# Performance work log

Measured on AMD Instinct MI355X. Metric: run time of the kernel, lower is better.

The kernel has to match this reference:

```python
import jax, jax.numpy as jnp
import numpy as np

B, N, C, H, P = 8, 4096, 256, 4, 64  # batch, tokens, hidden, heads, proj_size


def setup_inputs() -> dict:
    key = jax.random.key(0)
    ks = jax.random.split(key, 6)
    sc = 0.02
    x = jax.random.normal(ks[0], (B, N, C), jnp.float32)
    bank = jax.random.normal(ks[1], (B, N, C), jnp.float32)  # unused by forward, kept for fidelity
    W_qkvv = jax.random.normal(ks[2], (4 * C, C), jnp.float32) * sc  # Linear(C, 4C), no bias
    W_E = jax.random.normal(ks[3], (P, N), jnp.float32) * sc          # E = F shared Linear(N, P)
    b_E = jnp.zeros((P,), jnp.float32)
    temperature = jnp.ones((H, 1, 1), jnp.float32)
    temperature2 = jnp.ones((H, 1, 1), jnp.float32)
    W_out1 = jax.random.normal(ks[4], (C // 2, C), jnp.float32) * sc  # out_proj (spatial branch)
    b_out1 = jnp.zeros((C // 2,), jnp.float32)
    W_out2 = jax.random.normal(ks[5], (C // 2, C), jnp.float32) * sc  # out_proj2 (channel branch)
    b_out2 = jnp.zeros((C // 2,), jnp.float32)
    prelu_a = jnp.array(0.25, jnp.float32)  # nn.PReLU() default: single shared slope
    return {"x": x, "bank": bank, "W_qkvv": W_qkvv, "W_E": W_E, "b_E": b_E,
            "temperature": temperature, "temperature2": temperature2,
            "W_out1": W_out1, "b_out1": b_out1, "W_out2": W_out2, "b_out2": b_out2,
            "prelu_a": prelu_a}


def _l2norm(t):
    # torch F.normalize(dim=-1): x / max(||x||_2, eps)
    return t / jnp.maximum(jnp.linalg.norm(t, axis=-1, keepdims=True), 1e-12)


def reference(x, bank, W_qkvv, W_E, b_E, temperature, temperature2,
              W_out1, b_out1, W_out2, b_out2, prelu_a):
    Bb, Nn, Cc = x.shape
    Hh = temperature.shape[0]
    d = Cc // Hh
    # qkvv projection -> [4, B, H, N, d], then transpose token/feature axes -> [B, H, d, N]
    qkvv = (x @ W_qkvv.T).reshape(Bb, Nn, 4, Hh, d).transpose(2, 0, 3, 1, 4)
    q, k, v_ca, v_sa = (qkvv[0].transpose(0, 1, 3, 2), qkvv[1].transpose(0, 1, 3, 2),
                        qkvv[2].transpose(0, 1, 3, 2), qkvv[3].transpose(0, 1, 3, 2))
    # shared linear E=F projects the token axis N -> P (applied to UNnormalized k, v_sa)
    k_proj = jnp.einsum('bhdn,pn->bhdp', k, W_E) + b_E      # [B,H,d,P]
    v_sa_proj = jnp.einsum('bhdn,pn->bhdp', v_sa, W_E) + b_E  # [B,H,d,P]
    qn = _l2norm(q)
    kn = _l2norm(k)
    # channel attention: [B,H,d,d]
    attn_ca = jax.nn.softmax(jnp.einsum('bhdn,bhen->bhde', qn, kn) * temperature, axis=-1)
    x_ca = jnp.einsum('bhde,bhen->bhdn', attn_ca, v_ca).transpose(0, 3, 1, 2).reshape(Bb, Nn, Cc)
    # spatial attention (projected): [B,H,N,P]
    attn_sa = jax.nn.softmax(jnp.einsum('bhdn,bhdp->bhnp', qn, k_proj) * temperature2, axis=-1)
    x_sa = jnp.einsum('bhnp,bhdp->bhnd', attn_sa, v_sa_proj).transpose(0, 2, 1, 3).reshape(Bb, Nn, Cc)
    x_sa = x_sa @ W_out1.T + b_out1
    x_ca = x_ca @ W_out2.T + b_out2
    out = jnp.concatenate([x_sa, x_ca], axis=-1)
    return jnp.where(out >= 0, out, prelu_a * out)  # PReLU
```

## Files before the change

kernel.cpp:

```cpp
#include <hip/hip_runtime.h>
#include <cstdint>
#include <cstddef>

constexpr int B_ = 8, N_ = 4096, C_ = 256, H_ = 4, D_ = 64, P_ = 64;
constexpr int OC_ = 4 * C_;
constexpr int M_  = B_ * N_;
constexpr int GX_ROWS = 320;
constexpr int KSPLIT_G = 16;

#define DEV_INLINE __device__ __forceinline__

typedef unsigned short ushort_t;
typedef __attribute__((ext_vector_type(8))) short short8;
typedef __attribute__((ext_vector_type(4))) short short4v;
typedef __attribute__((ext_vector_type(4))) float floatx4;

DEV_INLINE short f2bf(float f) {
  unsigned int u = __builtin_bit_cast(unsigned int, f);
  u += 0x7FFFu + ((u >> 16) & 1u);
  return (short)(u >> 16);
}
DEV_INLINE float bf2f(ushort_t u) {
  return __builtin_bit_cast(float, (unsigned int)u << 16);
}
DEV_INLINE short4v cvt4(float4 v) {
  short4v s = {f2bf(v.x), f2bf(v.y), f2bf(v.z), f2bf(v.w)};
  return s;
}

__global__ __launch_bounds__(512) void k_qv(const float* __restrict__ x,
                                            const float* __restrict__ Wq,
                                            const float* __restrict__ WE,
                                            const float* __restrict__ W1,
                                            const float* __restrict__ W2,
                                            ushort_t* __restrict__ xb,
                                            ushort_t* __restrict__ wqb,
                                            ushort_t* __restrict__ web,
                                            ushort_t* __restrict__ w1b,
                                            ushort_t* __restrict__ w2b,
                                            ushort_t* __restrict__ qv) {
  __shared__ __align__(16) short As[128 * 72];
  __shared__ __align__(16) short Bs[256 * 72];
  const int cs = blockIdx.y;
  const int t = threadIdx.x;
  if (cs == 2) {
    constexpr size_t WQ4 = 65536, WE4 = 65536, W14 = 8192;
    constexpr size_t TOTW4 = WQ4 + WE4 + 2 * W14;
    for (size_t i = (size_t)blockIdx.x * 512 + t; i < TOTW4; i += (size_t)256 * 512) {
      const float* src; ushort_t* dst; size_t o;
      if (i < WQ4) { src = Wq; dst = wqb; o = i; }
      else if (i < WQ4 + WE4) { src = WE; dst = web; o = i - WQ4; }
      else if (i < WQ4 + WE4 + W14) { src = W1; dst = w1b; o = i - WQ4 - WE4; }
      else { src = W2; dst = w2b; o = i - WQ4 - WE4 - W14; }
      float4 v = ((const float4*)src)[o];
      *(short4v*)&dst[o * 4] = cvt4(v);
    }
    return;
  }
  const int bm = blockIdx.x * 128;
  const int wbase = cs ? 512 : 0;
  const int c = (t & 15) * 4;
  const int row = t >> 4;
  const int lane = t & 63, wave = t >> 6;
  const int m16 = lane & 15, quad = lane >> 4;
  const int wm = (wave >> 2) << 6, wn = (wave & 3) << 6;
  floatx4 acc[4][4];
#pragma unroll
  for (int i = 0; i < 4; ++i)
#pragma unroll
    for (int j = 0; j < 4; ++j) acc[i][j] = (floatx4)(0.f);
#pragma unroll 1
  for (int k0 = 0; k0 < 256; k0 += 64) {
    float4 av[4], bv[8];
#pragma unroll
    for (int rep = 0; rep < 4; ++rep)
      av[rep] = *(const float4*)&x[(size_t)(bm + row + 32 * rep) * 256 + k0 + c];
#pragma unroll
    for (int rep = 0; rep < 8; ++rep)
      bv[rep] = *(const float4*)&Wq[(size_t)(wbase + row + 32 * rep) * 256 + k0 + c];
    __syncthreads();
#pragma unroll
    for (int rep = 0; rep < 4; ++rep) {
      short4v s = cvt4(av[rep]);
      *(short4v*)&As[(row + 32 * rep) * 72 + c] = s;
      if (cs == 0)
        *(short4v*)&xb[(size_t)(bm + row + 32 * rep) * 256 + k0 + c] = s;
    }
#pragma unroll
    for (int rep = 0; rep < 8; ++rep)
      *(short4v*)&Bs[(row + 32 * rep) * 72 + c] = cvt4(bv[rep]);
    __syncthreads();
#pragma unroll
    for (int ks = 0; ks < 2; ++ks) {
      short8 af[4], bf[4];
#pragma unroll
      for (int i = 0; i < 4; ++i)
        af[i] = *(const short8*)&As[(wm + i * 16 + m16) * 72 + ks * 32 + quad * 8];
#pragma unroll
      for (int j = 0; j < 4; ++j)
        bf[j] = *(const short8*)&Bs[(wn + j * 16 + m16) * 72 + ks * 32 + quad * 8];
#pragma unroll
      for (int i = 0; i < 4; ++i)
#pragma unroll
        for (int j = 0; j < 4; ++j)
          acc[i][j] = __builtin_amdgcn_mfma_f32_16x16x32_bf16(af[i], bf[j], acc[i][j], 0, 0, 0);
    }
  }
#pragma unroll
  for (int i = 0; i < 4; ++i)
#pragma unroll
    for (int r = 0; r < 4; ++r) {
      const int gr = bm + wm + i * 16 + quad * 4 + r;
#pragma unroll
      for (int j = 0; j < 4; ++j)
        qv[(size_t)gr * 512 + cs * 256 + wn + j * 16 + m16] =
            (ushort_t)f2bf(acc[i][j][r]);
    }
}

__global__ __launch_bounds__(512) void k_gram(const ushort_t* __restrict__ xb,
                                              const ushort_t* __restrict__ web,
                                              float* __restrict__ Gx) {
  __shared__ __align__(16) short Bs[256 * 64];
  __shared__ __align__(16) short Ws[64 * 64];
  const int job = blockIdx.x;
  const int b = blockIdx.y >> 4;
  const int ksp = blockIdx.y & 15;
  const int t = threadIdx.x;
  const int lane = t & 63, wave = t >> 6;
  const int m16 = lane & 15, quad = lane >> 4;
  const int wm = (wave >> 2) << 6;
  const int wn4 = (wave & 3) << 6;
  const int wn2 = wave << 5;
  const int c0 = (t & 63) * 4;
  const int tp = t >> 6;
  floatx4 acc[4][4];
#pragma unroll
  for (int i = 0; i < 4; ++i)
#pragma unroll
    for (int j = 0; j < 4; ++j) acc[i][j] = (floatx4)(0.f);
#pragma unroll 1
  for (int it = 0; it < 4; ++it) {
    const int n0 = ksp * (N_ / KSPLIT_G) + it * 64;
    __syncthreads();
#pragma unroll
    for (int q = 0; q < 4; ++q) {
      const int tok = q * 16 + 2 * tp;
      const size_t r0 = (size_t)(b * N_ + n0 + tok) * C_ + c0;
      short4v aa = *(const short4v*)&xb[r0];
      short4v cc = *(const short4v*)&xb[r0 + C_];
#pragma unroll
      for (int ii = 0; ii < 4; ++ii) {
        const int r = c0 + ii;
        const int col = tok ^ (8 * ((r >> 3) & 7));
        unsigned int w = (unsigned int)(ushort_t)aa[ii] |
                         ((unsigned int)(ushort_t)cc[ii] << 16);
        *(unsigned int*)&Bs[r * 64 + col] = w;
      }
    }
    if (job == 2) {
      const int oc8 = (t & 7) * 8;
      const int p0 = t >> 3;
      short8 v = *(const short8*)&web[(size_t)p0 * N_ + n0 + oc8];
      *(short8*)&Ws[p0 * 64 + (oc8 ^ (8 * ((p0 >> 3) & 7)))] = v;
    }
    __syncthreads();
#pragma unroll
    for (int ks = 0; ks < 2; ++ks) {
      const int boct = ks * 32 + quad * 8;
      if (job < 2) {
        short8 af[4], bf[4];
#pragma unroll
        for (int i = 0; i < 4; ++i) {
          const int rA = job * 128 + wm + 16 * i + m16;
          af[i] = *(const short8*)&Bs[rA * 64 + (boct ^ (8 * ((rA >> 3) & 7)))];
        }
#pragma unroll
        for (int j = 0; j < 4; ++j) {
          const int rB = wn4 + 16 * j + m16;
          bf[j] = *(const short8*)&Bs[rB * 64 + (boct ^ (8 * ((rB >> 3) & 7)))];
        }
#pragma unroll
        for (int i = 0; i < 4; ++i)
#pragma unroll
          for (int j = 0; j < 4; ++j)
            acc[i][j] = __builtin_amdgcn_mfma_f32_16x16x32_bf16(af[i], bf[j], acc[i][j], 0, 0, 0);
      } else {
        short8 af[4], bf[2];
#pragma unroll
        for (int i = 0; i < 4; ++i) {
          const int rA = 16 * i + m16;
          af[i] = *(const short8*)&Ws[rA * 64 + (boct ^ (8 * ((rA >> 3) & 7)))];
        }
#pragma unroll
        for (int j = 0; j < 2; ++j) {
          const int rB = wn2 + 16 * j + m16;
          bf[j] = *(const short8*)&Bs[rB * 64 + (boct ^ (8 * ((rB >> 3) & 7)))];
        }
#pragma unroll
        for (int i = 0; i < 4; ++i)
#pragma unroll
          for (int j = 0; j < 2; ++j)
            acc[i][j] = __builtin_amdgcn_mfma_f32_16x16x32_bf16(af[i], bf[j], acc[i][j], 0, 0, 0);
      }
    }
  }
  if (job < 2) {
#pragma unroll
    for (int i = 0; i < 4; ++i)
#pragma unroll
      for (int r = 0; r < 4; ++r) {
        const int grow = job * 128 + wm + 16 * i + quad * 4 + r;
        const size_t rowoff = ((size_t)b * GX_ROWS + grow) * 256;
#pragma unroll
        for (int j = 0; j < 4; ++j)
          atomicAdd(&Gx[rowoff + wn4 + 16 * j + m16], acc[i][j][r]);
      }
  } else {
#pragma unroll
    for (int i = 0; i < 4; ++i)
#pragma unroll
      for (int r = 0; r < 4; ++r) {
        const int grow = 256 + 16 * i + quad * 4 + r;
        const size_t rowoff = ((size_t)b * GX_ROWS + grow) * 256;
#pragma unroll
        for (int j = 0; j < 2; ++j)
          atomicAdd(&Gx[rowoff + wn2 + 16 * j + m16], acc[i][j][r]);
      }
  }
}

__global__ __launch_bounds__(256) void k_mid1(const ushort_t* __restrict__ wqb,
                                              const float* __restrict__ Gx,
                                              ushort_t* __restrict__ T2b,
                                              float* __restrict__ ssq) {
  __shared__ __align__(16) short As[128 * 72];
  __shared__ __align__(16) short Bs[128 * 72];
  const int bm = blockIdx.x * 128;
  const int b  = blockIdx.y >> 1;
  const int jb = blockIdx.y & 1;
  const int t = threadIdx.x;
  const int oc = t & 7;
  const int rr = t >> 3;
  const int lane = t & 63, wave = t >> 6;
  const int m16 = lane & 15, quad = lane >> 4;
  const int wm = (wave >> 1) << 6, wn = (wave & 1) << 6;
  const float* Bsrc = Gx + ((size_t)b * GX_ROWS + jb * 128) * 256;
  floatx4 acc[4][4];
#pragma unroll
  for (int i = 0; i < 4; ++i)
#pragma unroll
    for (int j = 0; j < 4; ++j) acc[i][j] = (floatx4)(0.f);
#pragma unroll 1
  for (int k0 = 0; k0 < 256; k0 += 64) {
    short8 a8[4], b8[4];
#pragma unroll
    for (int j = 0; j < 4; ++j) {
      const int r = rr + 32 * j;
      a8[j] = *(const short8*)&wqb[(size_t)(bm + r) * 256 + k0 + 8 * oc];
      float4 g0 = *(const float4*)&Bsrc[(size_t)r * 256 + k0 + 8 * oc];
      float4 g1 = *(const float4*)&Bsrc[(size_t)r * 256 + k0 + 8 * oc + 4];
      short8 bb;
      bb[0] = f2bf(g0.x); bb[1] = f2bf(g0.y); bb[2] = f2bf(g0.z); bb[3] = f2bf(g0.w);
      bb[4] = f2bf(g1.x); bb[5] = f2bf(g1.y); bb[6] = f2bf(g1.z); bb[7] = f2bf(g1.w);
      b8[j] = bb;
    }
    __syncthreads();
#pragma unroll
    for (int j = 0; j < 4; ++j) {
      const int r = rr + 32 * j;
      *(short8*)&As[r * 72 + 8 * oc] = a8[j];
      *(short8*)&Bs[r * 72 + 8 * oc] = b8[j];
    }
    __syncthreads();
#pragma unroll
    for (int ks = 0; ks < 2; ++ks) {
      short8 af[4], bf[4];
#pragma unroll
      for (int i = 0; i < 4; ++i)
        af[i] = *(const short8*)&As[(wm + i * 16 + m16) * 72 + ks * 32 + quad * 8];
#pragma unroll
      for (int j = 0; j < 4; ++j)
        bf[j] = *(const short8*)&Bs[(wn + j * 16 + m16) * 72 + ks * 32 + quad * 8];
#pragma unroll
      for (int i = 0; i < 4; ++i)
#pragma unroll
        for (int j = 0; j < 4; ++j)
          acc[i][j] = __builtin_amdgcn_mfma_f32_16x16x32_bf16(af[i], bf[j], acc[i][j], 0, 0, 0);
    }
  }
#pragma unroll
  for (int i = 0; i < 4; ++i)
#pragma unroll
    for (int r = 0; r < 4; ++r) {
      const int gr = bm + wm + i * 16 + quad * 4 + r;
      float s = 0.f;
#pragma unroll
      for (int j = 0; j < 4; ++j) {
        const int col = jb * 128 + wn + j * 16 + m16;
        T2b[((size_t)b * 512 + gr) * 256 + col] = (ushort_t)f2bf(acc[i][j][r]);
        s += bf2f(wqb[(size_t)gr * 256 + col]) * acc[i][j][r];
      }
      s += __shfl_xor(s, 1);
      s += __shfl_xor(s, 2);
      s += __shfl_xor(s, 4);
      s += __shfl_xor(s, 8);
      if (m16 == 0) atomicAdd(&ssq[b * 512 + gr], s);
    }
}

__global__ __launch_bounds__(64) void k_mid2(const ushort_t* __restrict__ wqb,
                                             const ushort_t* __restrict__ T2b,
                                             const float* __restrict__ Gx,
                                             const float* __restrict__ ssq,
                                             const float* __restrict__ bE,
                                             const float* __restrict__ t1,
                                             const float* __restrict__ t2,
                                             ushort_t* __restrict__ ab,
                                             ushort_t* __restrict__ ksb,
                                             ushort_t* __restrict__ vsb) {
  const int bh = blockIdx.x;
  const int job = blockIdx.y;
  const int b = bh >> 2, h = bh & 3;
  const int lane = threadIdx.x & 63;
  const int m16 = lane & 15, quad = lane >> 4;
  const int Abase = (job == 0 ? 0 : (job == 1 ? 256 : 768)) + h * 64;
  floatx4 acc[4][4];
#pragma unroll
  for (int i = 0; i < 4; ++i)
#pragma unroll
    for (int j = 0; j < 4; ++j) acc[i][j] = (floatx4)(0.f);
#pragma unroll
  for (int ks = 0; ks < 8; ++ks) {
    const int boct = ks * 32 + quad * 8;
    short8 af[4], bf[4];
#pragma unroll
    for (int i = 0; i < 4; ++i)
      af[i] = *(const short8*)&wqb[(size_t)(Abase + 16 * i + m16) * 256 + boct];
    if (job == 0) {
#pragma unroll
      for (int j = 0; j < 4; ++j)
        bf[j] = *(const short8*)&T2b[((size_t)b * 512 + 256 + h * 64 + 16 * j + m16) * 256 + boct];
    } else {
#pragma unroll
      for (int j = 0; j < 4; ++j) {
        const float* gp = Gx + ((size_t)b * GX_ROWS + 256 + 16 * j + m16) * 256 + boct;
        float4 g0 = *(const float4*)gp;
        float4 g1 = *(const float4*)(gp + 4);
        short8 bb;
        bb[0] = f2bf(g0.x); bb[1] = f2bf(g0.y); bb[2] = f2bf(g0.z); bb[3] = f2bf(g0.w);
        bb[4] = f2bf(g1.x); bb[5] = f2bf(g1.y); bb[6] = f2bf(g1.z); bb[7] = f2bf(g1.w);
        bf[j] = bb;
      }
    }
#pragma unroll
    for (int i = 0; i < 4; ++i)
#pragma unroll
      for (int j = 0; j < 4; ++j)
        acc[i][j] = __builtin_amdgcn_mfma_f32_16x16x32_bf16(af[i], bf[j], acc[i][j], 0, 0, 0);
  }
  if (job == 0) {
    const float t1h = t1[h];
    float rnk[4];
#pragma unroll
    for (int j = 0; j < 4; ++j)
      rnk[j] = 1.f / fmaxf(sqrtf(ssq[b * 512 + 256 + h * 64 + 16 * j + m16]), 1e-12f);
#pragma unroll
    for (int i = 0; i < 4; ++i)
#pragma unroll
      for (int r = 0; r < 4; ++r) {
        const int d = 16 * i + quad * 4 + r;
        const float rq = 1.f / fmaxf(sqrtf(ssq[b * 512 + h * 64 + d]), 1e-12f);
        float l[4];
        float m = -1e30f;
#pragma unroll
        for (int j = 0; j < 4; ++j) {
          l[j] = acc[i][j][r] * rq * rnk[j] * t1h;
          m = fmaxf(m, l[j]);
        }
        m = fmaxf(m, __shfl_xor(m, 1));
        m = fmaxf(m, __shfl_xor(m, 2));
        m = fmaxf(m, __shfl_xor(m, 4));
        m = fmaxf(m, __shfl_xor(m, 8));
        float s = 0.f;
#pragma unroll
        for (int j = 0; j < 4; ++j) {
          l[j] = __expf(l[j] - m);
          s += l[j];
        }
        s += __shfl_xor(s, 1);
        s += __shfl_xor(s, 2);
        s += __shfl_xor(s, 4);
        s += __shfl_xor(s, 8);
        const float inv = 1.f / s;
#pragma unroll
        for (int j = 0; j < 4; ++j)
          ab[(size_t)bh * 4096 + d * 64 + 16 * j + m16] = (ushort_t)f2bf(l[j] * inv);
      }
  } else if (job == 1) {
    const float tt = t2[h];
#pragma unroll
    for (int i = 0; i < 4; ++i)
#pragma unroll
      for (int r = 0; r < 4; ++r) {
        const int d = 16 * i + quad * 4 + r;
        const float rq = 1.f / fmaxf(sqrtf(ssq[b * 512 + h * 64 + d]), 1e-12f);
#pragma unroll
        for (int j = 0; j < 4; ++j) {
          const int p = 16 * j + m16;
          ksb[(size_t)bh * 4096 + p * 64 + d] =
              (ushort_t)f2bf((acc[i][j][r] + bE[p]) * rq * tt);
        }
      }
  } else {
#pragma unroll
    for (int i = 0; i < 4; ++i)
#pragma unroll
      for (int r = 0; r < 4; ++r) {
        const int d = 16 * i + quad * 4 + r;
#pragma unroll
        for (int j = 0; j < 4; ++j) {
          const int p = 16 * j + m16;
          vsb[(size_t)bh * 4096 + d * 64 + p] = (ushort_t)f2bf(acc[i][j][r] + bE[p]);
        }
      }
  }
}

__global__ __launch_bounds__(256) void k_attn(const ushort_t* __restrict__ qv,
                                              const ushort_t* __restrict__ ab,
                                              const ushort_t* __restrict__ ksb,
                                              const ushort_t* __restrict__ vsb,
                                              ushort_t* __restrict__ x_ca,
                                              ushort_t* __restrict__ x_sa) {
  __shared__ float Pl[64][68];
  const int bh = blockIdx.x;
  const int b = bh >> 2, h = bh & 3;
  const int lane = threadIdx.x & 63, wave = threadIdx.x >> 6;
  const int m16 = lane & 15, quad = lane >> 4;
  if (blockIdx.y < 32) {
    const int n0 = blockIdx.y * 128;
    const ushort_t* abb = ab + (size_t)bh * 4096;
    short8 bf[2][4];
#pragma unroll
    for (int ks = 0; ks < 2; ++ks)
#pragma unroll
      for (int j = 0; j < 4; ++j)
        bf[ks][j] = *(const short8*)&abb[(16 * j + m16) * 64 + ks * 32 + quad * 8];
#pragma unroll
    for (int mm = 0; mm < 2; ++mm) {
      const int tokbase = n0 + 64 * mm + 16 * wave;
      const ushort_t* vrow =
          qv + (size_t)(b * N_ + tokbase + m16) * 512 + 256 + h * 64 + quad * 8;
      short8 af0 = *(const short8*)&vrow[0];
      short8 af1 = *(const short8*)&vrow[32];
      floatx4 o[4];
#pragma unroll
      for (int j = 0; j < 4; ++j) o[j] = (floatx4)(0.f);
#pragma unroll
      for (int j = 0; j < 4; ++j) {
        o[j] = __builtin_amdgcn_mfma_f32_16x16x32_bf16(af0, bf[0][j], o[j], 0, 0, 0);
        o[j] = __builtin_amdgcn_mfma_f32_16x16x32_bf16(af1, bf[1][j], o[j], 0, 0, 0);
      }
#pragma unroll
      for (int j = 0; j < 4; ++j)
#pragma unroll
        for (int r = 0; r < 4; ++r)
          x_ca[(size_t)(b * N_ + tokbase + quad * 4 + r) * C_ + h * 64 + 16 * j + m16] =
              (ushort_t)f2bf(o[j][r]);
    }
    return;
  }
  const int n0 = (blockIdx.y - 32) * 64;
  const ushort_t* qrow =
      qv + (size_t)(b * N_ + n0 + 16 * wave + m16) * 512 + h * 64 + quad * 8;
  short8 qf0 = *(const short8*)&qrow[0];
  short8 qf1 = *(const short8*)&qrow[32];
  const ushort_t* kb = ksb + (size_t)bh * 4096;
  const ushort_t* vb = vsb + (size_t)bh * 4096;
  short8 kf[2][4], vf[2][4];
#pragma unroll
  for (int ks = 0; ks < 2; ++ks)
#pragma unroll
    for (int j = 0; j < 4; ++j) {
      kf[ks][j] = *(const short8*)&kb[(16 * j + m16) * 64 + ks * 32 + quad * 8];
      vf[ks][j] = *(const short8*)&vb[(16 * j + m16) * 64 + ks * 32 + quad * 8];
    }
  floatx4 s[4];
#pragma unroll
  for (int j = 0; j < 4; ++j) s[j] = (floatx4)(0.f);
#pragma unroll
  for (int j = 0; j < 4; ++j) {
    s[j] = __builtin_amdgcn_mfma_f32_16x16x32_bf16(qf0, kf[0][j], s[j], 0, 0, 0);
    s[j] = __builtin_amdgcn_mfma_f32_16x16x32_bf16(qf1, kf[1][j], s[j], 0, 0, 0);
  }
  float p[4][4];
#pragma unroll
  for (int r = 0; r < 4; ++r) {
    float mr = fmaxf(fmaxf(s[0][r], s[1][r]), fmaxf(s[2][r], s[3][r]));
    mr = fmaxf(mr, __shfl_xor(mr, 1));
    mr = fmaxf(mr, __shfl_xor(mr, 2));
    mr = fmaxf(mr, __shfl_xor(mr, 4));
    mr = fmaxf(mr, __shfl_xor(mr, 8));
    float sr = 0.f;
#pragma unroll
    for (int j = 0; j < 4; ++j) {
      const float e = __expf(s[j][r] - mr);
      p[j][r] = e;
      sr += e;
    }
    sr += __shfl_xor(sr, 1);
    sr += __shfl_xor(sr, 2);
    sr += __shfl_xor(sr, 4);
    sr += __shfl_xor(sr, 8);
    const float inv = 1.f / sr;
#pragma unroll
    for (int j = 0; j < 4; ++j) p[j][r] *= inv;
  }
#pragma unroll
  for (int j = 0; j < 4; ++j)
#pragma unroll
    for (int r = 0; r < 4; ++r)
      Pl[16 * wave + quad * 4 + r][16 * j + m16] = p[j][r];
  __syncthreads();
  short8 pf[2];
#pragma unroll
  for (int ks = 0; ks < 2; ++ks) {
    float4 x0 = *(const float4*)&Pl[16 * wave + m16][ks * 32 + quad * 8];
    float4 x1 = *(const float4*)&Pl[16 * wave + m16][ks * 32 + quad * 8 + 4];
    short8 v;
    v[0] = f2bf(x0.x); v[1] = f2bf(x0.y); v[2] = f2bf(x0.z); v[3] = f2bf(x0.w);
    v[4] = f2bf(x1.x); v[5] = f2bf(x1.y); v[6] = f2bf(x1.z); v[7] = f2bf(x1.w);
    pf[ks] = v;
  }
  floatx4 o[4];
#pragma unroll
  for (int j = 0; j < 4; ++j) o[j] = (floatx4)(0.f);
#pragma unroll
  for (int j = 0; j < 4; ++j) {
    o[j] = __builtin_amdgcn_mfma_f32_16x16x32_bf16(pf[0], vf[0][j], o[j], 0, 0, 0);
    o[j] = __builtin_amdgcn_mfma_f32_16x16x32_bf16(pf[1], vf[1][j], o[j], 0, 0, 0);
  }
#pragma unroll
  for (int j = 0; j < 4; ++j)
#pragma unroll
    for (int r = 0; r < 4; ++r)
      x_sa[(size_t)(b * N_ + n0 + 16 * wave + quad * 4 + r) * C_ + h * 64 + 16 * j + m16] =
          (ushort_t)f2bf(o[j][r]);
}

__global__ __launch_bounds__(256) void k_out_mfma(const ushort_t* __restrict__ xsa,
                                                  const ushort_t* __restrict__ xca,
                                                  const ushort_t* __restrict__ w1b,
                                                  const float* __restrict__ b1,
                                                  const ushort_t* __restrict__ w2b,
                                                  const float* __restrict__ b2,
                                                  const float* __restrict__ pa,
                                                  float* __restrict__ out) {
  __shared__ __align__(16) short As[128 * 72];
  __shared__ __align__(16) short Bs[128 * 72];
  const int bm = blockIdx.x * 128;
  const int half = blockIdx.y;
  const ushort_t* A = half ? xca : xsa;
  const ushort_t* W = half ? w2b : w1b;
  const float* bias = half ? b2 : b1;
  const int t = threadIdx.x;
  const int oc = t & 7;
  const int rr = t >> 3;
  const int lane = t & 63, wave = t >> 6;
  const int m16 = lane & 15, quad = lane >> 4;
  const int wm = (wave >> 1) << 6, wn = (wave & 1) << 6;
  floatx4 acc[4][4];
#pragma unroll
  for (int i = 0; i < 4; ++i)
#pragma unroll
    for (int j = 0; j < 4; ++j) acc[i][j] = (floatx4)(0.f);
#pragma unroll 1
  for (int k0 = 0; k0 < 256; k0 += 64) {
    short8 a8[4], b8[4];
#pragma unroll
    for (int j = 0; j < 4; ++j) {
      const int r = rr + 32 * j;
      a8[j] = *(const short8*)&A[(size_t)(bm + r) * 256 + k0 + 8 * oc];
      b8[j] = *(const short8*)&W[(size_t)r * 256 + k0 + 8 * oc];
    }
    __syncthreads();
#pragma unroll
    for (int j = 0; j < 4; ++j) {
      const int r = rr + 32 * j;
      *(short8*)&As[r * 72 + 8 * oc] = a8[j];
      *(short8*)&Bs[r * 72 + 8 * oc] = b8[j];
    }
    __syncthreads();
#pragma unroll
    for (int ks = 0; ks < 2; ++ks) {
      short8 af[4], bf[4];
#pragma unroll
      for (int i = 0; i < 4; ++i)
        af[i] = *(const short8*)&As[(wm + i * 16 + m16) * 72 + ks * 32 + quad * 8];
#pragma unroll
      for (int j = 0; j < 4; ++j)
        bf[j] = *(const short8*)&Bs[(wn + j * 16 + m16) * 72 + ks * 32 + quad * 8];
#pragma unroll
      for (int i = 0; i < 4; ++i)
#pragma unroll
        for (int j = 0; j < 4; ++j)
          acc[i][j] = __builtin_amdgcn_mfma_f32_16x16x32_bf16(af[i], bf[j], acc[i][j], 0, 0, 0);
    }
  }
  const float slope = pa[0];
  float bj[4];
#pragma unroll
  for (int j = 0; j < 4; ++j) bj[j] = bias[wn + j * 16 + m16];
#pragma unroll
  for (int i = 0; i < 4; ++i)
#pragma unroll
    for (int r = 0; r < 4; ++r) {
      const int gr = bm + wm + i * 16 + quad * 4 + r;
#pragma unroll
      for (int j = 0; j < 4; ++j) {
        float v = acc[i][j][r] + bj[j];
        v = v >= 0.f ? v : slope * v;
        out[(size_t)gr * C_ + half * 128 + wn + j * 16 + m16] = v;
      }
    }
}

extern "C" void kernel_launch(void* const* d_in, const int* in_sizes, int n_in,
                              void* d_out, int out_size, void* d_ws, size_t ws_size,
                              hipStream_t stream) {
  (void)in_sizes; (void)n_in; (void)out_size; (void)ws_size;
  const float* x  = (const float*)d_in[0];
  const float* Wq = (const float*)d_in[2];
  const float* WE = (const float*)d_in[3];
  const float* bE = (const float*)d_in[4];
  const float* t1 = (const float*)d_in[5];
  const float* t2 = (const float*)d_in[6];
  const float* W1 = (const float*)d_in[7];
  const float* b1 = (const float*)d_in[8];
  const float* W2 = (const float*)d_in[9];
  const float* b2 = (const float*)d_in[10];
  const float* pa = (const float*)d_in[11];
  float* out = (float*)d_out;

  float* ws = (float*)d_ws;
  size_t off = 0;
  float* Gx  = ws + off; off += (size_t)B_ * GX_ROWS * 256;
  float* ssq = ws + off; off += (size_t)B_ * 512;
  ushort_t* qv  = (ushort_t*)(ws + off); off += (size_t)M_ * 512 / 2;
  ushort_t* xsa = (ushort_t*)(ws + off); off += (size_t)M_ * C_ / 2;
  ushort_t* xca = (ushort_t*)(ws + off); off += (size_t)M_ * C_ / 2;
  ushort_t* ksb = (ushort_t*)(ws + off); off += 32 * 4096 / 2;
  ushort_t* vsb = (ushort_t*)(ws + off); off += 32 * 4096 / 2;
  ushort_t* ab  = (ushort_t*)(ws + off); off += 32 * 4096 / 2;
  ushort_t* xb  = (ushort_t*)(ws + off); off += (size_t)M_ * C_ / 2;
  ushort_t* wqb = (ushort_t*)(ws + off); off += (size_t)OC_ * C_ / 2;
  ushort_t* w1b = (ushort_t*)(ws + off); off += (size_t)128 * C_ / 2;
  ushort_t* w2b = (ushort_t*)(ws + off); off += (size_t)128 * C_ / 2;
  ushort_t* web = (ushort_t*)(ws + off); off += (size_t)P_ * N_ / 2;
  ushort_t* T2b = (ushort_t*)(ws + off); off += (size_t)B_ * 512 * C_ / 2;

  hipMemsetAsync(Gx, 0, ((size_t)B_ * GX_ROWS * 256 + B_ * 512) * sizeof(float), stream);

  k_qv<<<dim3(M_ / 128, 3), 512, 0, stream>>>(x, Wq, WE, W1, W2,
                                              xb, wqb, web, w1b, w2b, qv);
  k_gram<<<dim3(3, B_ * KSPLIT_G), 512, 0, stream>>>(xb, web, Gx);
  k_mid1<<<dim3(4, B_ * 2), 256, 0, stream>>>(wqb, Gx, T2b, ssq);
  k_mid2<<<dim3(32, 3), 64, 0, stream>>>(wqb, T2b, Gx, ssq, bE, t1, t2, ab, ksb, vsb);
  k_attn<<<dim3(32, 96), 256, 0, stream>>>(qv, ab, ksb, vsb, xca, xsa);
  k_out_mfma<<<dim3(M_ / 128, 2), 256, 0, stream>>>(xsa, xca, w1b, b1, w2b, b2, pa, out);
}
```

Before: 255.8 us.

## Split cast/transpose kernel, use transposed bf16 x for gram, replace atomics with partial reduction

Adds a separate cast kernel that converts x to bf16 and also writes a channel-major transposed copy, plus converts the weights. The qv GEMM and gram GEMM then read bf16 directly with 16-byte loads instead of converting fp32 or doing in-LDS transposes. Gram split-K now writes per-split partials that a new reduction kernel sums, replacing global float atomics and the large memset. The cost is an extra kernel launch, an extra full bf16 copy of x written and read, and a larger workspace for the partials.

```diff
diff --git a/kernel.cpp b/kernel.cpp
--- a/kernel.cpp
+++ b/kernel.cpp
@@ -6,7 +6,8 @@
 constexpr int OC_ = 4 * C_;
 constexpr int M_  = B_ * N_;
 constexpr int GX_ROWS = 320;
-constexpr int KSPLIT_G = 16;
+constexpr int KS_G = 8;
+constexpr int XT_TILES = M_ / 64;
 
 #define DEV_INLINE __device__ __forceinline__
 
@@ -28,25 +29,25 @@
   return s;
 }
 
-__global__ __launch_bounds__(512) void k_qv(const float* __restrict__ x,
-                                            const float* __restrict__ Wq,
-                                            const float* __restrict__ WE,
-                                            const float* __restrict__ W1,
-                                            const float* __restrict__ W2,
-                                            ushort_t* __restrict__ xb,
-                                            ushort_t* __restrict__ wqb,
-                                            ushort_t* __restrict__ web,
-                                            ushort_t* __restrict__ w1b,
-                                            ushort_t* __restrict__ w2b,
-                                            ushort_t* __restrict__ qv) {
-  __shared__ __align__(16) short As[128 * 72];
-  __shared__ __align__(16) short Bs[256 * 72];
-  const int cs = blockIdx.y;
+__global__ __launch_bounds__(256) void k_cast(const float* __restrict__ x,
+                                              const float* __restrict__ Wq,
+                                              const float* __restrict__ WE,
+                                              const float* __restrict__ W1,
+                                              const float* __restrict__ W2,
+                                              ushort_t* __restrict__ xb,
+                                              ushort_t* __restrict__ xt,
+                                              ushort_t* __restrict__ wqb,
+                                              ushort_t* __restrict__ web,
+                                              ushort_t* __restrict__ w1b,
+                                              ushort_t* __restrict__ w2b) {
   const int t = threadIdx.x;
-  if (cs == 2) {
-    constexpr size_t WQ4 = 65536, WE4 = 65536, W14 = 8192;
+  if (blockIdx.x >= XT_TILES) {
+    constexpr size_t WQ4 = (size_t)OC_ * C_ / 4;
+    constexpr size_t WE4 = (size_t)P_ * N_ / 4;
+    constexpr size_t W14 = (size_t)128 * C_ / 4;
     constexpr size_t TOTW4 = WQ4 + WE4 + 2 * W14;
-    for (size_t i = (size_t)blockIdx.x * 512 + t; i < TOTW4; i += (size_t)256 * 512) {
+    const size_t stride = (size_t)128 * 256;
+    for (size_t i = (size_t)(blockIdx.x - XT_TILES) * 256 + t; i < TOTW4; i += stride) {
       const float* src; ushort_t* dst; size_t o;
       if (i < WQ4) { src = Wq; dst = wqb; o = i; }
       else if (i < WQ4 + WE4) { src = WE; dst = web; o = i - WQ4; }
@@ -57,10 +58,40 @@
     }
     return;
   }
+  __shared__ __align__(16) short Xs[64 * 264];
+  const int n0 = blockIdx.x * 64;
+  const int b = n0 >> 12, nl = n0 & 4095;
+#pragma unroll
+  for (int rep = 0; rep < 16; ++rep) {
+    const int f4 = rep * 256 + t;
+    const int row = f4 >> 6, c4 = f4 & 63;
+    float4 v = *(const float4*)&x[(size_t)(n0 + row) * 256 + c4 * 4];
+    short4v s = cvt4(v);
+    *(short4v*)&xb[(size_t)(n0 + row) * 256 + c4 * 4] = s;
+    *(short4v*)&Xs[row * 264 + c4 * 4] = s;
+  }
+  __syncthreads();
+  const int ch = t;
+  ushort_t* dst = &xt[((size_t)b * 256 + ch) * 4096 + nl];
+#pragma unroll
+  for (int g = 0; g < 8; ++g) {
+    short8 o;
+#pragma unroll
+    for (int i = 0; i < 8; ++i) o[i] = Xs[(g * 8 + i) * 264 + ch];
+    *(short8*)&dst[g * 8] = o;
+  }
+}
+
+__global__ __launch_bounds__(512) void k_qv(const ushort_t* __restrict__ xb,
+                                            const ushort_t* __restrict__ wqb,
+                                            ushort_t* __restrict__ qv) {
+  __shared__ __align__(16) short As[128 * 72];
+  __shared__ __align__(16) short Bs[256 * 72];
   const int bm = blockIdx.x * 128;
-  const int wbase = cs ? 512 : 0;
-  const int c = (t & 15) * 4;
-  const int row = t >> 4;
+  const int y = blockIdx.y;
+  const int wrow = y ? 512 : 0;
+  const int t = threadIdx.x;
+  const int oc = t & 7, rr = t >> 3;
   const int lane = t & 63, wave = t >> 6;
   const int m16 = lane & 15, quad = lane >> 4;
   const int wm = (wave >> 2) << 6, wn = (wave & 3) << 6;
@@ -71,24 +102,20 @@
     for (int j = 0; j < 4; ++j) acc[i][j] = (floatx4)(0.f);
 #pragma unroll 1
   for (int k0 = 0; k0 < 256; k0 += 64) {
-    float4 av[4], bv[8];
-#pragma unroll
-    for (int rep = 0; rep < 4; ++rep)
-      av[rep] = *(const float4*)&x[(size_t)(bm + row + 32 * rep) * 256 + k0 + c];
-#pragma unroll
-    for (int rep = 0; rep < 8; ++rep)
-      bv[rep] = *(const float4*)&Wq[(size_t)(wbase + row + 32 * rep) * 256 + k0 + c];
+    short8 a8[2], b8[4];
+#pragma unroll
+    for (int rp = 0; rp < 2; ++rp)
+      a8[rp] = *(const short8*)&xb[(size_t)(bm + rr + 64 * rp) * 256 + k0 + 8 * oc];
+#pragma unroll
+    for (int rp = 0; rp < 4; ++rp)
+      b8[rp] = *(const short8*)&wqb[(size_t)(wrow + rr + 64 * rp) * 256 + k0 + 8 * oc];
     __syncthreads();
 #pragma unroll
-    for (int rep = 0; rep < 4; ++rep) {
-      short4v s = cvt4(av[rep]);
-      *(short4v*)&As[(row + 32 * rep) * 72 + c] = s;
-      if (cs == 0)
-        *(short4v*)&xb[(size_t)(bm + row + 32 * rep) * 256 + k0 + c] = s;
-    }
-#pragma unroll
-    for (int rep = 0; rep < 8; ++rep)
-      *(short4v*)&Bs[(row + 32 * rep) * 72 + c] = cvt4(bv[rep]);
+    for (int rp = 0; rp < 2; ++rp)
+      *(short8*)&As[(rr + 64 * rp) * 72 + 8 * oc] = a8[rp];
+#pragma unroll
+    for (int rp = 0; rp < 4; ++rp)
+      *(short8*)&Bs[(rr + 64 * rp) * 72 + 8 * oc] = b8[rp];
     __syncthreads();
 #pragma unroll
     for (int ks = 0; ks < 2; ++ks) {
@@ -113,73 +140,63 @@
       const int gr = bm + wm + i * 16 + quad * 4 + r;
 #pragma unroll
       for (int j = 0; j < 4; ++j)
-        qv[(size_t)gr * 512 + cs * 256 + wn + j * 16 + m16] =
+        qv[(size_t)gr * 512 + y * 256 + wn + j * 16 + m16] =
             (ushort_t)f2bf(acc[i][j][r]);
     }
 }
 
-__global__ __launch_bounds__(512) void k_gram(const ushort_t* __restrict__ xb,
+__global__ __launch_bounds__(512) void k_gram(const ushort_t* __restrict__ xt,
                                               const ushort_t* __restrict__ web,
-                                              float* __restrict__ Gx) {
-  __shared__ __align__(16) short Bs[256 * 64];
-  __shared__ __align__(16) short Ws[64 * 64];
+                                              float* __restrict__ Gxp) {
+  __shared__ __align__(16) short As[128 * 72];
+  __shared__ __align__(16) short Bs[256 * 72];
   const int job = blockIdx.x;
-  const int b = blockIdx.y >> 4;
-  const int ksp = blockIdx.y & 15;
+  const int y = blockIdx.y;
+  const int b = y >> 3, ksp = y & 7;
   const int t = threadIdx.x;
+  const int oc = t & 7, rr = t >> 3;
   const int lane = t & 63, wave = t >> 6;
   const int m16 = lane & 15, quad = lane >> 4;
-  const int wm = (wave >> 2) << 6;
-  const int wn4 = (wave & 3) << 6;
-  const int wn2 = wave << 5;
-  const int c0 = (t & 63) * 4;
-  const int tp = t >> 6;
+  const int wm = (wave >> 2) << 6, wn = (wave & 3) << 6;
+  const ushort_t* Asrc = (job < 2)
+      ? xt + (size_t)(b * 256 + job * 128) * 4096 : web;
+  const ushort_t* Bsrc = xt + (size_t)b * 256 * 4096;
   floatx4 acc[4][4];
 #pragma unroll
   for (int i = 0; i < 4; ++i)
 #pragma unroll
     for (int j = 0; j < 4; ++j) acc[i][j] = (floatx4)(0.f);
 #pragma unroll 1
-  for (int it = 0; it < 4; ++it) {
-    const int n0 = ksp * (N_ / KSPLIT_G) + it * 64;
+  for (int it = 0; it < 8; ++it) {
+    const int n0 = ksp * 512 + it * 64;
+    short8 a8[2], b8[4];
+#pragma unroll
+    for (int rp = 0; rp < 2; ++rp) {
+      int ar = rr + 64 * rp;
+      if (job == 2) ar &= 63;
+      a8[rp] = *(const short8*)&Asrc[(size_t)ar * 4096 + n0 + 8 * oc];
+    }
+#pragma unroll
+    for (int rp = 0; rp < 4; ++rp)
+      b8[rp] = *(const short8*)&Bsrc[(size_t)(rr + 64 * rp) * 4096 + n0 + 8 * oc];
     __syncthreads();
 #pragma unroll
-    for (int q = 0; q < 4; ++q) {
-      const int tok = q * 16 + 2 * tp;
-      const size_t r0 = (size_t)(b * N_ + n0 + tok) * C_ + c0;
-      short4v aa = *(const short4v*)&xb[r0];
-      short4v cc = *(const short4v*)&xb[r0 + C_];
-#pragma unroll
-      for (int ii = 0; ii < 4; ++ii) {
-        const int r = c0 + ii;
-        const int col = tok ^ (8 * ((r >> 3) & 7));
-        unsigned int w = (unsigned int)(ushort_t)aa[ii] |
-                         ((unsigned int)(ushort_t)cc[ii] << 16);
-        *(unsigned int*)&Bs[r * 64 + col] = w;
-      }
-    }
-    if (job == 2) {
-      const int oc8 = (t & 7) * 8;
-      const int p0 = t >> 3;
-      short8 v = *(const short8*)&web[(size_t)p0 * N_ + n0 + oc8];
-      *(short8*)&Ws[p0 * 64 + (oc8 ^ (8 * ((p0 >> 3) & 7)))] = v;
-    }
+    for (int rp = 0; rp < 2; ++rp)
+      *(short8*)&As[(rr + 64 * rp) * 72 + 8 * oc] = a8[rp];
+#pragma unroll
+    for (int rp = 0; rp < 4; ++rp)
+      *(short8*)&Bs[(rr + 64 * rp) * 72 + 8 * oc] = b8[rp];
     __syncthreads();
 #pragma unroll
     for (int ks = 0; ks < 2; ++ks) {
-      const int boct = ks * 32 + quad * 8;
       if (job < 2) {
         short8 af[4], bf[4];
 #pragma unroll
-        for (int i = 0; i < 4; ++i) {
-          const int rA = job * 128 + wm + 16 * i + m16;
-          af[i] = *(const short8*)&Bs[rA * 64 + (boct ^ (8 * ((rA >> 3) & 7)))];
-        }
-#pragma unroll
-        for (int j = 0; j < 4; ++j) {
-          const int rB = wn4 + 16 * j + m16;
-          bf[j] = *(const short8*)&Bs[rB * 64 + (boct ^ (8 * ((rB >> 3) & 7)))];
-        }
+        for (int i = 0; i < 4; ++i)
+          af[i] = *(const short8*)&As[(wm + i * 16 + m16) * 72 + ks * 32 + quad * 8];
+#pragma unroll
+        for (int j = 0; j < 4; ++j)
+          bf[j] = *(const short8*)&Bs[(wn + j * 16 + m16) * 72 + ks * 32 + quad * 8];
 #pragma unroll
         for (int i = 0; i < 4; ++i)
 #pragma unroll
@@ -188,15 +205,11 @@
       } else {
         short8 af[4], bf[2];
 #pragma unroll
-        for (int i = 0; i < 4; ++i) {
-          const int rA = 16 * i + m16;
-          af[i] = *(const short8*)&Ws[rA * 64 + (boct ^ (8 * ((rA >> 3) & 7)))];
-        }
-#pragma unroll
-        for (int j = 0; j < 2; ++j) {
-          const int rB = wn2 + 16 * j + m16;
-          bf[j] = *(const short8*)&Bs[rB * 64 + (boct ^ (8 * ((rB >> 3) & 7)))];
-        }
+        for (int i = 0; i < 4; ++i)
+          af[i] = *(const short8*)&As[(i * 16 + m16) * 72 + ks * 32 + quad * 8];
+#pragma unroll
+        for (int j = 0; j < 2; ++j)
+          bf[j] = *(const short8*)&Bs[(wave * 32 + j * 16 + m16) * 72 + ks * 32 + quad * 8];
 #pragma unroll
         for (int i = 0; i < 4; ++i)
 #pragma unroll
@@ -205,29 +218,43 @@
       }
     }
   }
+  float* pb = Gxp + (size_t)y * (GX_ROWS * 256);
   if (job < 2) {
 #pragma unroll
     for (int i = 0; i < 4; ++i)
 #pragma unroll
       for (int r = 0; r < 4; ++r) {
-        const int grow = job * 128 + wm + 16 * i + quad * 4 + r;
-        const size_t rowoff = ((size_t)b * GX_ROWS + grow) * 256;
+        const int grow = job * 128 + wm + i * 16 + quad * 4 + r;
 #pragma unroll
         for (int j = 0; j < 4; ++j)
-          atomicAdd(&Gx[rowoff + wn4 + 16 * j + m16], acc[i][j][r]);
+          pb[(size_t)grow * 256 + wn + j * 16 + m16] = acc[i][j][r];
       }
   } else {
 #pragma unroll
     for (int i = 0; i < 4; ++i)
 #pragma unroll
       for (int r = 0; r < 4; ++r) {
-        const int grow = 256 + 16 * i + quad * 4 + r;
-        const size_t rowoff = ((size_t)b * GX_ROWS + grow) * 256;
+        const int grow = 256 + i * 16 + quad * 4 + r;
 #pragma unroll
         for (int j = 0; j < 2; ++j)
-          atomicAdd(&Gx[rowoff + wn2 + 16 * j + m16], acc[i][j][r]);
-      }
-  }
+          pb[(size_t)grow * 256 + wave * 32 + j * 16 + m16] = acc[i][j][r];
+      }
+  }
+}
+
+__global__ __launch_bounds__(256) void k_gred(const float* __restrict__ Gxp,
+                                              float* __restrict__ Gx) {
+  const int i = blockIdx.x * 256 + threadIdx.x;
+  constexpr int PB4 = GX_ROWS * 256 / 4;
+  const int fb = i / PB4, rem = i - fb * PB4;
+  const float4* p = (const float4*)Gxp;
+  float4 s = p[(size_t)fb * KS_G * PB4 + rem];
+#pragma unroll
+  for (int k = 1; k < KS_G; ++k) {
+    float4 v = p[((size_t)fb * KS_G + k) * PB4 + rem];
+    s.x += v.x; s.y += v.y; s.z += v.z; s.w += v.w;
+  }
+  ((float4*)Gx)[i] = s;
 }
 
 __global__ __launch_bounds__(256) void k_mid1(const ushort_t* __restrict__ wqb,
@@ -647,6 +674,7 @@
   size_t off = 0;
   float* Gx  = ws + off; off += (size_t)B_ * GX_ROWS * 256;
   float* ssq = ws + off; off += (size_t)B_ * 512;
+  float* Gxp = ws + off; off += (size_t)KS_G * B_ * GX_ROWS * 256;
   ushort_t* qv  = (ushort_t*)(ws + off); off += (size_t)M_ * 512 / 2;
   ushort_t* xsa = (ushort_t*)(ws + off); off += (size_t)M_ * C_ / 2;
   ushort_t* xca = (ushort_t*)(ws + off); off += (size_t)M_ * C_ / 2;
@@ -654,17 +682,20 @@
   ushort_t* vsb = (ushort_t*)(ws + off); off += 32 * 4096 / 2;
   ushort_t* ab  = (ushort_t*)(ws + off); off += 32 * 4096 / 2;
   ushort_t* xb  = (ushort_t*)(ws + off); off += (size_t)M_ * C_ / 2;
+  ushort_t* xt  = (ushort_t*)(ws + off); off += (size_t)M_ * C_ / 2;
   ushort_t* wqb = (ushort_t*)(ws + off); off += (size_t)OC_ * C_ / 2;
   ushort_t* w1b = (ushort_t*)(ws + off); off += (size_t)128 * C_ / 2;
   ushort_t* w2b = (ushort_t*)(ws + off); off += (size_t)128 * C_ / 2;
   ushort_t* web = (ushort_t*)(ws + off); off += (size_t)P_ * N_ / 2;
   ushort_t* T2b = (ushort_t*)(ws + off); off += (size_t)B_ * 512 * C_ / 2;
 
-  hipMemsetAsync(Gx, 0, ((size_t)B_ * GX_ROWS * 256 + B_ * 512) * sizeof(float), stream);
-
-  k_qv<<<dim3(M_ / 128, 3), 512, 0, stream>>>(x, Wq, WE, W1, W2,
-                                              xb, wqb, web, w1b, w2b, qv);
-  k_gram<<<dim3(3, B_ * KSPLIT_G), 512, 0, stream>>>(xb, web, Gx);
+  hipMemsetAsync(ssq, 0, (size_t)B_ * 512 * sizeof(float), stream);
+
+  k_cast<<<XT_TILES + 128, 256, 0, stream>>>(x, Wq, WE, W1, W2,
+                                             xb, xt, wqb, web, w1b, w2b);
+  k_qv<<<dim3(M_ / 128, 2), 512, 0, stream>>>(xb, wqb, qv);
+  k_gram<<<dim3(3, B_ * KS_G), 512, 0, stream>>>(xt, web, Gxp);
+  k_gred<<<GX_ROWS * 256 * B_ / 4 / 256, 256, 0, stream>>>(Gxp, Gx);
   k_mid1<<<dim3(4, B_ * 2), 256, 0, stream>>>(wqb, Gx, T2b, ssq);
   k_mid2<<<dim3(32, 3), 64, 0, stream>>>(wqb, T2b, Gx, ssq, bE, t1, t2, ab, ksb, vsb);
   k_attn<<<dim3(32, 96), 256, 0, stream>>>(qv, ab, ksb, vsb, xca, xsa);
```

Measured after the change: 240.8 us. -5.8%, faster.
